# Optimization experiments

Measured on AMD Instinct MI355X. Metric: run time of the kernel, lower is better.

The kernel has to match this reference:

```python
import jax, jax.numpy as jnp
import numpy as np

D_MODEL = 2048
N_HEADS = 16
D_HEAD = D_MODEL // N_HEADS
B, S = 4, 2048


def setup_inputs() -> dict:
    key = jax.random.key(0)
    ks = jax.random.split(key, 5)
    scale = 1.0 / np.sqrt(D_MODEL)
    return {
        "x": jax.random.normal(ks[0], (B, S, D_MODEL), dtype=jnp.float32),
        "w_qkv": jax.random.normal(ks[1], (D_MODEL, 3 * D_MODEL), dtype=jnp.float32) * scale,
        "b_qkv": jax.random.normal(ks[2], (3 * D_MODEL,), dtype=jnp.float32) * 0.01,
        "w_out": jax.random.normal(ks[3], (D_MODEL, D_MODEL), dtype=jnp.float32) * scale,
        "b_out": jax.random.normal(ks[4], (D_MODEL,), dtype=jnp.float32) * 0.01,
    }


def reference(x, w_qkv, b_qkv, w_out, b_out):
    b, s, d = x.shape
    qkv = x @ w_qkv + b_qkv                      # [b, s, 3d]
    q, k, v = jnp.split(qkv, 3, axis=-1)
    # [b, h, s, dh]
    q = q.reshape(b, s, N_HEADS, D_HEAD).transpose(0, 2, 1, 3)
    k = k.reshape(b, s, N_HEADS, D_HEAD).transpose(0, 2, 1, 3)
    v = v.reshape(b, s, N_HEADS, D_HEAD).transpose(0, 2, 1, 3)
    # past_kv is None -> s_past == s
    scale = 1.0 / np.sqrt(D_HEAD).astype(np.float32)
    scores = jnp.einsum("bhqd,bhkd->bhqk", q, k) * scale  # [b, h, s, s]
    # causal mask: disallow j > i (diagonal = 1 + s_past - s = 1)
    causal = jnp.tril(jnp.ones((s, s), dtype=bool))
    scores = jnp.where(causal, scores, jnp.float32(-jnp.inf))
    attn = jax.nn.softmax(scores, axis=-1)
    out = jnp.einsum("bhqk,bhkd->bhqd", attn, v)          # [b, h, s, dh]
    out = out.transpose(0, 2, 1, 3).reshape(b, s, d)
    out = out @ w_out + b_out
    return out, k, v
```

## Files before the change

kernel.cpp:

```cpp
#include <hip/hip_runtime.h>
#include <hip/hip_bf16.h>
#include <cstdint>

typedef unsigned short u16;
typedef unsigned int u32;
typedef __attribute__((ext_vector_type(4))) float f32x4;
typedef __attribute__((ext_vector_type(8))) __bf16 bf16x8;

#define DEVFN static __device__ __forceinline__

constexpr int Bb = 4, S = 2048, Dm = 2048, H = 16, DH = 128;
constexpr int M  = Bb * S;
constexpr int N3 = 3 * Dm;
constexpr int KK = 2048;
constexpr float ATTN_SCALE = 0.088388347648318447f;
constexpr float LOG2E = 1.4426950408889634f;

DEVFN u16 f2bf(float f) {
  union { float f; u32 u; } v; v.f = f;
  u32 u = v.u;
  return (u16)((u + 0x7fffu + ((u >> 16) & 1u)) >> 16);
}

DEVFN void async16(const void* g, void* l) {
  __builtin_amdgcn_global_load_lds(
      (__attribute__((address_space(1))) unsigned int*)(g),
      (__attribute__((address_space(3))) unsigned int*)(l), 16, 0, 0);
}


__global__ __launch_bounds__(256) void k_cvt_bf16(const float* __restrict__ in,
                                                  u16* __restrict__ out, int n) {
  int i = (blockIdx.x * 256 + threadIdx.x) * 4;
  if (i < n) {
    float4 f = *(const float4*)(in + i);
    ushort4 o;
    o.x = f2bf(f.x); o.y = f2bf(f.y); o.z = f2bf(f.z); o.w = f2bf(f.w);
    *(ushort4*)(out + i) = o;
  }
}

__global__ __launch_bounds__(256) void k_transpose_bf16(const float* __restrict__ in,
                                                        u16* __restrict__ out,
                                                        int R, int C) {
  __shared__ float tile[32][33];
  int c0 = blockIdx.x * 32, r0 = blockIdx.y * 32;
  int tx = threadIdx.x & 31, ty = threadIdx.x >> 5;
#pragma unroll
  for (int i = 0; i < 4; i++)
    tile[ty + 8 * i][tx] = in[(size_t)(r0 + ty + 8 * i) * C + c0 + tx];
  __syncthreads();
#pragma unroll
  for (int i = 0; i < 4; i++)
    out[(size_t)(c0 + ty + 8 * i) * R + r0 + tx] = f2bf(tile[tx][ty + 8 * i]);
}


#define RA(buf, half) ((buf) * 65536 + (half) * 16384)
#define RB(buf, half) ((buf) * 65536 + 32768 + (half) * 16384)

#define BARRIER() __builtin_amdgcn_s_barrier()
#define LGKM12() { asm volatile("s_waitcnt lgkmcnt(12)" ::: "memory"); __builtin_amdgcn_sched_barrier(0); }
#define LGKM0()  { asm volatile("s_waitcnt lgkmcnt(0)" ::: "memory"); __builtin_amdgcn_sched_barrier(0); }
#define VMC4()   { asm volatile("s_waitcnt vmcnt(4)" ::: "memory"); __builtin_amdgcn_sched_barrier(0); }
#define VMC8()   { asm volatile("s_waitcnt vmcnt(8)" ::: "memory"); __builtin_amdgcn_sched_barrier(0); }
#define VMC0()   { asm volatile("s_waitcnt vmcnt(0)" ::: "memory"); __builtin_amdgcn_sched_barrier(0); }

template <int BUF, int QUAD>
DEVFN void ldAq(const char* lds, int wm, int lrow, int lkg, bf16x8 af[4][2]) {
  const char* base = lds + RA(BUF, 0) + wm * 16384;
  const int sw = (lrow & 7) << 4;
#pragma unroll
  for (int mi = 0; mi < 4; mi++) {
    int row = QUAD * 64 + mi * 16 + lrow;
#pragma unroll
    for (int kk = 0; kk < 2; kk++)
      af[mi][kk] = *(const bf16x8*)(base + row * 128 + ((kk * 64 + lkg * 16) ^ sw));
  }
}

template <int BUF, int NS>
DEVFN void ldB(const char* lds, int wn, int lrow, int lkg, bf16x8 b[2][2]) {
  const char* base = lds + RB(BUF, 0) + (wn >> 1) * 16384;
  const int sw = (lrow & 7) << 4;
#pragma unroll
  for (int ni = 0; ni < 2; ni++) {
    int row = (wn & 1) * 64 + NS * 32 + ni * 16 + lrow;
#pragma unroll
    for (int kk = 0; kk < 2; kk++)
      b[ni][kk] = *(const bf16x8*)(base + row * 128 + ((kk * 64 + lkg * 16) ^ sw));
  }
}

template <int MS, int NS>
DEVFN void mmq(f32x4 acc[8][4], bf16x8 af[4][2], bf16x8 b[2][2]) {
  __builtin_amdgcn_s_setprio(1);
#pragma unroll
  for (int kk = 0; kk < 2; kk++)
#pragma unroll
    for (int mi = 0; mi < 4; mi++)
#pragma unroll
      for (int ni = 0; ni < 2; ni++)
        acc[MS * 4 + mi][NS * 2 + ni] = __builtin_amdgcn_mfma_f32_16x16x32_bf16(
            af[mi][kk], b[ni][kk], acc[MS * 4 + mi][NS * 2 + ni], 0, 0, 0);
  __builtin_amdgcn_s_setprio(0);
}

DEVFN void stage2(const u16* src, char* ldsc, int region, int dstoff) {
  async16(src, ldsc + region + dstoff);
  async16(src + (size_t)64 * KK, ldsc + region + 8192 + dstoff);
}

template <int MODE>
__global__ __launch_bounds__(512, 2) void k_gemm(
    const u16* __restrict__ A, const u16* __restrict__ BT,
    const float* __restrict__ bias, float* __restrict__ Cf,
    u16* __restrict__ q_bf, u16* __restrict__ k_bf, u16* __restrict__ v_bfT,
    int N) {
  __shared__ __align__(16) char lds[131072];
  char* ldsc = lds;
  const int tid = threadIdx.x;
  const int wid = tid >> 6, lane = tid & 63;
  const int wm = wid >> 2, wn = wid & 3;
  const int lrow = lane & 15, lkg = lane >> 4;

  const int bid = blockIdx.x;
  const int xcd = bid & 7;
  const int i = bid >> 3;
  const int r = i & 15;
  const int j = i >> 4;
  const int tm0 = (xcd * 4 + (r >> 2)) << 8;
  const int tn0 = (j * 4 + (r & 3)) << 8;

  const int NT = KK >> 6;

  const int srow = tid >> 3;
  const int scol = (((tid & 7) * 16) ^ ((srow & 7) << 4)) >> 1;
  const int dstoff = (tid & ~63) * 16;
  const u16* bA0 = A + (size_t)(tm0 + srow) * KK + scol;
  const u16* bA1 = A + (size_t)(tm0 + 128 + srow) * KK + scol;
  const u16* bB0 = BT + (size_t)(tn0 + srow) * KK + scol;
  const u16* bB1 = BT + (size_t)(tn0 + 128 + srow) * KK + scol;

  f32x4 acc[8][4] = {};
  bf16x8 afX[4][2], afY[4][2], bX[2][2], bY[2][2];

  stage2(bA0, ldsc, RA(0, 0), dstoff);
  stage2(bA1, ldsc, RA(0, 1), dstoff);
  stage2(bB0, ldsc, RB(0, 0), dstoff);
  stage2(bB1, ldsc, RB(0, 1), dstoff);
  stage2(bA0 + 64, ldsc, RA(1, 0), dstoff);
  stage2(bA1 + 64, ldsc, RA(1, 1), dstoff);
  stage2(bB0 + 64, ldsc, RB(1, 0), dstoff);
  stage2(bB1 + 64, ldsc, RB(1, 1), dstoff);
  VMC8();
  BARRIER();
  ldAq<0, 0>(ldsc, wm, lrow, lkg, afX);
  ldB<0, 0>(ldsc, wn, lrow, lkg, bX);

  for (int it = 0; it < NT / 2; it++) {
    const int u = it * 2;
    const int t2 = (u + 2 < NT) ? u + 2 : NT - 2;
    const int t3 = (u + 3 < NT) ? u + 3 : NT - 1;

    ldAq<0, 1>(ldsc, wm, lrow, lkg, afY);
    ldB<0, 1>(ldsc, wn, lrow, lkg, bY);
    LGKM12();
    mmq<0, 0>(acc, afX, bX);
    LGKM0();
    BARRIER();

    stage2(bA0 + t2 * 64, ldsc, RA(0, 0), dstoff);
    stage2(bA1 + t2 * 64, ldsc, RA(0, 1), dstoff);
    mmq<0, 1>(acc, afX, bY);
    VMC4();
    BARRIER();

    ldAq<1, 0>(ldsc, wm, lrow, lkg, afX);
    stage2(bB0 + t2 * 64, ldsc, RB(0, 0), dstoff);
    mmq<1, 1>(acc, afY, bY);
    BARRIER();

    ldB<1, 0>(ldsc, wn, lrow, lkg, bY);
    stage2(bB1 + t2 * 64, ldsc, RB(0, 1), dstoff);
    mmq<1, 0>(acc, afY, bX);
    BARRIER();

    ldAq<1, 1>(ldsc, wm, lrow, lkg, afY);
    ldB<1, 1>(ldsc, wn, lrow, lkg, bX);
    LGKM12();
    mmq<0, 0>(acc, afX, bY);
    LGKM0();
    BARRIER();

    stage2(bA0 + t3 * 64, ldsc, RA(1, 0), dstoff);
    stage2(bA1 + t3 * 64, ldsc, RA(1, 1), dstoff);
    mmq<0, 1>(acc, afX, bX);
    VMC4();
    BARRIER();

    ldAq<0, 0>(ldsc, wm, lrow, lkg, afX);
    stage2(bB0 + t3 * 64, ldsc, RB(1, 0), dstoff);
    mmq<1, 1>(acc, afY, bX);
    BARRIER();

    ldB<0, 0>(ldsc, wn, lrow, lkg, bX);
    stage2(bB1 + t3 * 64, ldsc, RB(1, 1), dstoff);
    mmq<1, 0>(acc, afY, bY);
    BARRIER();
  }
  VMC0();
  LGKM0();

  if (MODE == 0) {
#pragma unroll
    for (int mig = 0; mig < 8; mig++) {
      int row = tm0 + wm * 128 + (mig >> 2) * 64 + (mig & 3) * 16 + lkg * 4;
#pragma unroll
      for (int nig = 0; nig < 4; nig++) {
        int col = tn0 + wn * 64 + (nig >> 1) * 32 + (nig & 1) * 16 + lrow;
        float bv = bias[col];
#pragma unroll
        for (int r2 = 0; r2 < 4; r2++)
          Cf[(size_t)(row + r2) * N + col] = acc[mig][nig][r2] + bv;
      }
    }
  } else {
#pragma unroll
    for (int mig = 0; mig < 8; mig++) {
      int row = tm0 + wm * 128 + (mig >> 2) * 64 + (mig & 3) * 16 + lkg * 4;
#pragma unroll
      for (int nig = 0; nig < 4; nig++) {
        int n = tn0 + wn * 64 + (nig >> 1) * 32 + (nig & 1) * 16 + lrow;
        float bv = bias[n];
        int type = n >> 11;
        int d = n & 2047;
        int h = d >> 7, dh = d & 127;
#pragma unroll
        for (int r2 = 0; r2 < 4; r2++) {
          int rr = row + r2;
          int b = rr >> 11, s = rr & 2047;
          float val = acc[mig][nig][r2] + bv;
          size_t idx = ((size_t)(b * H + h) * S + s) * DH + dh;
          if (type == 0) {
            q_bf[idx] = f2bf(val * ATTN_SCALE);
          } else if (type == 1) {
            Cf[(size_t)M * Dm + idx] = val;
            k_bf[idx] = f2bf(val);
          } else {
            Cf[(size_t)2 * M * Dm + idx] = val;
            v_bfT[((size_t)(b * H + h) * DH + dh) * S + s] = f2bf(val);
          }
        }
      }
    }
  }
}

__global__ __launch_bounds__(256, 2) void k_attn(const u16* __restrict__ q_bf,
                                                 const u16* __restrict__ k_bf,
                                                 const u16* __restrict__ v_bfT,
                                                 u16* __restrict__ attn_bf) {
  __shared__ u16 ldsK[2][64 * 128];
  __shared__ u16 ldsV[2][128 * 64];
  __shared__ u16 ldsP[4][32 * 64];

  const int tid = threadIdx.x;
  const int wid = tid >> 6, lane = tid & 63;
  const int lrow = lane & 15, lkg = lane >> 4;

  const int bid = blockIdx.x;
  const int xcd = bid & 7;
  const int ii = bid >> 3;
  const int bh = xcd * 8 + (ii >> 4);
  const int qi = 15 - (ii & 15);
  const int b = bh >> 4, h = bh & 15;
  const int wq0 = qi * 128 + wid * 32;
  const int swz = (lrow & 7) << 4;

  const u16* qp = q_bf + (size_t)bh * S * DH;
  const u16* kp = k_bf + (size_t)bh * S * DH;
  const u16* vp = v_bfT + (size_t)bh * DH * S;

  bf16x8 qf[2][4];
#pragma unroll
  for (int qt = 0; qt < 2; qt++)
#pragma unroll
    for (int kk = 0; kk < 4; kk++)
      qf[qt][kk] = *(const bf16x8*)(qp + (size_t)(wq0 + qt * 16 + lrow) * DH +
                                    kk * 32 + lkg * 8);

  float mr[2][4], lr[2][4];
#pragma unroll
  for (int qt = 0; qt < 2; qt++)
#pragma unroll
    for (int r = 0; r < 4; r++) { mr[qt][r] = -1e30f; lr[qt][r] = 0.f; }
  f32x4 oacc[2][8] = {};

  const int nkb = qi * 2 + 2;

  auto stage = [&](int kb, int buf) {
#pragma unroll
    for (int i = 0; i < 4; i++) {
      int L = i * 4096 + wid * 1024 + lane * 16;
      int krow = L >> 8, kch = (L >> 4) & 15;
      async16(kp + (size_t)(kb * 64 + krow) * DH + ((kch ^ (krow & 7)) * 8),
              (char*)ldsK[buf] + L);
      int vd = L >> 7, vch = (L >> 4) & 7;
      async16(vp + (size_t)vd * S + kb * 64 + ((vch ^ (vd & 7)) * 8),
              (char*)ldsV[buf] + L);
    }
  };

  stage(0, 0);
  asm volatile("s_waitcnt vmcnt(0)" ::: "memory");
  __builtin_amdgcn_s_barrier();

  int cur = 0;
  for (int kb = 0; kb < nkb; kb++) {
    if (kb + 1 < nkb) stage(kb + 1, cur ^ 1);

    if (kb * 64 <= wq0 + 31) {
      const u16* Kc = ldsK[cur];
      const u16* Vc = ldsV[cur];
      f32x4 sacc[2][4] = {};
      __builtin_amdgcn_s_setprio(1);
#pragma unroll
      for (int kt = 0; kt < 4; kt++)
#pragma unroll
        for (int kk = 0; kk < 4; kk++) {
          bf16x8 kf = *(const bf16x8*)((const char*)Kc +
                        (kt * 16 + lrow) * 256 + ((kk * 64 + lkg * 16) ^ swz));
          sacc[0][kt] = __builtin_amdgcn_mfma_f32_16x16x32_bf16(qf[0][kk], kf,
                                                                sacc[0][kt], 0, 0, 0);
          sacc[1][kt] = __builtin_amdgcn_mfma_f32_16x16x32_bf16(qf[1][kk], kf,
                                                                sacc[1][kt], 0, 0, 0);
        }
      __builtin_amdgcn_s_setprio(0);

      if (kb * 64 + 63 > wq0) {
#pragma unroll
        for (int qt = 0; qt < 2; qt++)
#pragma unroll
          for (int kt = 0; kt < 4; kt++) {
            int k = kb * 64 + kt * 16 + lrow;
#pragma unroll
            for (int r = 0; r < 4; r++)
              if (k > wq0 + qt * 16 + lkg * 4 + r) sacc[qt][kt][r] = -1e30f;
          }
      }

      float pm[2][4];
#pragma unroll
      for (int qt = 0; qt < 2; qt++)
#pragma unroll
        for (int r = 0; r < 4; r++)
          pm[qt][r] = fmaxf(fmaxf(sacc[qt][0][r], sacc[qt][1][r]),
                            fmaxf(sacc[qt][2][r], sacc[qt][3][r]));
#pragma unroll
      for (int off = 1; off < 16; off <<= 1)
#pragma unroll
        for (int qt = 0; qt < 2; qt++)
#pragma unroll
          for (int r = 0; r < 4; r++)
            pm[qt][r] = fmaxf(pm[qt][r], __shfl_xor(pm[qt][r], off, 64));

      float dmax = pm[0][0] - mr[0][0];
#pragma unroll
      for (int qt = 0; qt < 2; qt++)
#pragma unroll
        for (int r = 0; r < 4; r++)
          dmax = fmaxf(dmax, pm[qt][r] - mr[qt][r]);
      if (!__all(dmax <= 8.0f)) {
        float sc[2][4];
#pragma unroll
        for (int qt = 0; qt < 2; qt++)
#pragma unroll
          for (int r = 0; r < 4; r++) {
            float mn = fmaxf(mr[qt][r], pm[qt][r]);
            sc[qt][r] = exp2f((mr[qt][r] - mn) * LOG2E);
            mr[qt][r] = mn;
            lr[qt][r] *= sc[qt][r];
          }
#pragma unroll
        for (int qt = 0; qt < 2; qt++)
#pragma unroll
          for (int nd = 0; nd < 8; nd++)
#pragma unroll
            for (int r = 0; r < 4; r++) oacc[qt][nd][r] *= sc[qt][r];
      }

      float rs[2][4] = {};
#pragma unroll
      for (int qt = 0; qt < 2; qt++)
#pragma unroll
        for (int kt = 0; kt < 4; kt++)
#pragma unroll
          for (int r = 0; r < 4; r++) {
            float p = exp2f((sacc[qt][kt][r] - mr[qt][r]) * LOG2E);
            rs[qt][r] += p;
            int prow = qt * 16 + lkg * 4 + r;
            *(u16*)((char*)ldsP[wid] + prow * 128 +
                    (((kt * 16 + lrow) * 2) ^ ((prow & 7) << 4))) = f2bf(p);
          }
#pragma unroll
      for (int off = 1; off < 16; off <<= 1)
#pragma unroll
        for (int qt = 0; qt < 2; qt++)
#pragma unroll
          for (int r = 0; r < 4; r++)
            rs[qt][r] += __shfl_xor(rs[qt][r], off, 64);
#pragma unroll
      for (int qt = 0; qt < 2; qt++)
#pragma unroll
        for (int r = 0; r < 4; r++)
          lr[qt][r] += rs[qt][r];

      asm volatile("s_waitcnt lgkmcnt(0)" ::: "memory");
      bf16x8 pf[2][2];
#pragma unroll
      for (int qt = 0; qt < 2; qt++)
#pragma unroll
        for (int kk = 0; kk < 2; kk++)
          pf[qt][kk] = *(const bf16x8*)((const char*)ldsP[wid] +
                         (qt * 16 + lrow) * 128 + ((kk * 64 + lkg * 16) ^ swz));
      __builtin_amdgcn_s_setprio(1);
#pragma unroll
      for (int nd = 0; nd < 8; nd++) {
        bf16x8 vf0 = *(const bf16x8*)((const char*)Vc +
                       (nd * 16 + lrow) * 128 + ((lkg * 16) ^ swz));
        bf16x8 vf1 = *(const bf16x8*)((const char*)Vc +
                       (nd * 16 + lrow) * 128 + ((64 + lkg * 16) ^ swz));
#pragma unroll
        for (int qt = 0; qt < 2; qt++) {
          oacc[qt][nd] = __builtin_amdgcn_mfma_f32_16x16x32_bf16(pf[qt][0], vf0,
                                                                 oacc[qt][nd], 0, 0, 0);
          oacc[qt][nd] = __builtin_amdgcn_mfma_f32_16x16x32_bf16(pf[qt][1], vf1,
                                                                 oacc[qt][nd], 0, 0, 0);
        }
      }
      __builtin_amdgcn_s_setprio(0);
    }

    asm volatile("s_waitcnt vmcnt(0)" ::: "memory");
    __builtin_amdgcn_s_barrier();
    cur ^= 1;
  }

#pragma unroll
  for (int qt = 0; qt < 2; qt++) {
    float inv[4];
#pragma unroll
    for (int r = 0; r < 4; r++) inv[r] = 1.0f / lr[qt][r];
#pragma unroll
    for (int nd = 0; nd < 8; nd++)
#pragma unroll
      for (int r = 0; r < 4; r++) {
        int q = wq0 + qt * 16 + lkg * 4 + r;
        size_t idx = ((size_t)(b * S + q) * H + h) * DH + nd * 16 + lrow;
        attn_bf[idx] = f2bf(oacc[qt][nd][r] * inv[r]);
      }
  }
}


extern "C" void kernel_launch(void* const* d_in, const int* in_sizes, int n_in,
                              void* d_out, int out_size, void* d_ws, size_t ws_size,
                              hipStream_t stream) {
  const float* x     = (const float*)d_in[0];
  const float* w_qkv = (const float*)d_in[1];
  const float* b_qkv = (const float*)d_in[2];
  const float* w_out = (const float*)d_in[3];
  const float* b_out = (const float*)d_in[4];
  float* out = (float*)d_out;

  char* ws = (char*)d_ws;
  u16* x_bf    = (u16*)ws; ws += (size_t)M * Dm * 2;
  u16* wqkvT   = (u16*)ws; ws += (size_t)N3 * Dm * 2;
  u16* woutT   = (u16*)ws; ws += (size_t)Dm * Dm * 2;
  u16* q_bf    = (u16*)ws; ws += (size_t)M * Dm * 2;
  u16* k_bf    = (u16*)ws; ws += (size_t)M * Dm * 2;
  u16* v_bfT   = (u16*)ws; ws += (size_t)M * Dm * 2;
  u16* attn_bf = (u16*)ws; ws += (size_t)M * Dm * 2;

  k_cvt_bf16<<<(M * Dm) / 1024, 256, 0, stream>>>(x, x_bf, M * Dm);
  k_transpose_bf16<<<dim3(N3 / 32, Dm / 32), 256, 0, stream>>>(w_qkv, wqkvT, Dm, N3);
  k_transpose_bf16<<<dim3(Dm / 32, Dm / 32), 256, 0, stream>>>(w_out, woutT, Dm, Dm);

  k_gemm<1><<<(N3 / 256) * (M / 256), 512, 0, stream>>>(
      x_bf, wqkvT, b_qkv, out, q_bf, k_bf, v_bfT, N3);

  k_attn<<<S / 128 * Bb * H, 256, 0, stream>>>(q_bf, k_bf, v_bfT, attn_bf);

  k_gemm<0><<<(Dm / 256) * (M / 256), 512, 0, stream>>>(
      attn_bf, woutT, b_out, out, nullptr, nullptr, nullptr, Dm);
}
```

Baseline: 565.7 us.

## Restructure GEMM main loop into finer-grained quarter-tile staged pipeline

Rewrites the GEMM K-loop schedule so each global-to-LDS async load is issued one quarter-tile at a time, interleaved with eight MFMA phases per double iteration. It uses tighter vmcnt(2) waits and full lgkmcnt(0) waits between barrier pairs, instead of the previous lgkmcnt(12)/vmcnt(4) scheme with register prefetch across phases. The goal is smoother overlap of global loads with compute. The trade-off is many more barriers per iteration and less LDS-read to MFMA overlap, which could stall the waves.

```diff
diff --git a/kernel.cpp b/kernel.cpp
--- a/kernel.cpp
+++ b/kernel.cpp
@@ -60,11 +60,9 @@
 #define RB(buf, half) ((buf) * 65536 + 32768 + (half) * 16384)
 
 #define BARRIER() __builtin_amdgcn_s_barrier()
-#define LGKM12() { asm volatile("s_waitcnt lgkmcnt(12)" ::: "memory"); __builtin_amdgcn_sched_barrier(0); }
-#define LGKM0()  { asm volatile("s_waitcnt lgkmcnt(0)" ::: "memory"); __builtin_amdgcn_sched_barrier(0); }
-#define VMC4()   { asm volatile("s_waitcnt vmcnt(4)" ::: "memory"); __builtin_amdgcn_sched_barrier(0); }
-#define VMC8()   { asm volatile("s_waitcnt vmcnt(8)" ::: "memory"); __builtin_amdgcn_sched_barrier(0); }
-#define VMC0()   { asm volatile("s_waitcnt vmcnt(0)" ::: "memory"); __builtin_amdgcn_sched_barrier(0); }
+#define LGK0() { asm volatile("s_waitcnt lgkmcnt(0)" ::: "memory"); __builtin_amdgcn_sched_barrier(0); }
+#define VMC2() { asm volatile("s_waitcnt vmcnt(2)" ::: "memory"); __builtin_amdgcn_sched_barrier(0); }
+#define VMC0() { asm volatile("s_waitcnt vmcnt(0)" ::: "memory"); __builtin_amdgcn_sched_barrier(0); }
 
 template <int BUF, int QUAD>
 DEVFN void ldAq(const char* lds, int wm, int lrow, int lkg, bf16x8 af[4][2]) {
@@ -104,11 +102,6 @@
         acc[MS * 4 + mi][NS * 2 + ni] = __builtin_amdgcn_mfma_f32_16x16x32_bf16(
             af[mi][kk], b[ni][kk], acc[MS * 4 + mi][NS * 2 + ni], 0, 0, 0);
   __builtin_amdgcn_s_setprio(0);
-}
-
-DEVFN void stage2(const u16* src, char* ldsc, int region, int dstoff) {
-  async16(src, ldsc + region + dstoff);
-  async16(src + (size_t)64 * KK, ldsc + region + 8192 + dstoff);
 }
 
 template <int MODE>
@@ -142,75 +135,79 @@
   const u16* bB0 = BT + (size_t)(tn0 + srow) * KK + scol;
   const u16* bB1 = BT + (size_t)(tn0 + 128 + srow) * KK + scol;
 
+  auto stage2 = [&](const u16* src, int region) {
+    async16(src, ldsc + region + dstoff);
+    async16(src + (size_t)64 * KK, ldsc + region + 8192 + dstoff);
+  };
+
   f32x4 acc[8][4] = {};
-  bf16x8 afX[4][2], afY[4][2], bX[2][2], bY[2][2];
-
-  stage2(bA0, ldsc, RA(0, 0), dstoff);
-  stage2(bA1, ldsc, RA(0, 1), dstoff);
-  stage2(bB0, ldsc, RB(0, 0), dstoff);
-  stage2(bB1, ldsc, RB(0, 1), dstoff);
-  stage2(bA0 + 64, ldsc, RA(1, 0), dstoff);
-  stage2(bA1 + 64, ldsc, RA(1, 1), dstoff);
-  stage2(bB0 + 64, ldsc, RB(1, 0), dstoff);
-  stage2(bB1 + 64, ldsc, RB(1, 1), dstoff);
-  VMC8();
+  bf16x8 afA[4][2], afB[4][2], b0[2][2], b1[2][2];
+
+  stage2(bA0, RA(0, 0));
+  stage2(bA1, RA(0, 1));
+  stage2(bB0, RB(0, 0));
+  stage2(bB1, RB(0, 1));
+  stage2(bA0 + 64, RA(1, 0));
+  VMC2();
   BARRIER();
-  ldAq<0, 0>(ldsc, wm, lrow, lkg, afX);
-  ldB<0, 0>(ldsc, wn, lrow, lkg, bX);
 
   for (int it = 0; it < NT / 2; it++) {
-    const int u = it * 2;
-    const int t2 = (u + 2 < NT) ? u + 2 : NT - 2;
-    const int t3 = (u + 3 < NT) ? u + 3 : NT - 1;
-
-    ldAq<0, 1>(ldsc, wm, lrow, lkg, afY);
-    ldB<0, 1>(ldsc, wn, lrow, lkg, bY);
-    LGKM12();
-    mmq<0, 0>(acc, afX, bX);
-    LGKM0();
-    BARRIER();
-
-    stage2(bA0 + t2 * 64, ldsc, RA(0, 0), dstoff);
-    stage2(bA1 + t2 * 64, ldsc, RA(0, 1), dstoff);
-    mmq<0, 1>(acc, afX, bY);
-    VMC4();
-    BARRIER();
-
-    ldAq<1, 0>(ldsc, wm, lrow, lkg, afX);
-    stage2(bB0 + t2 * 64, ldsc, RB(0, 0), dstoff);
-    mmq<1, 1>(acc, afY, bY);
-    BARRIER();
-
-    ldB<1, 0>(ldsc, wn, lrow, lkg, bY);
-    stage2(bB1 + t2 * 64, ldsc, RB(0, 1), dstoff);
-    mmq<1, 0>(acc, afY, bX);
-    BARRIER();
-
-    ldAq<1, 1>(ldsc, wm, lrow, lkg, afY);
-    ldB<1, 1>(ldsc, wn, lrow, lkg, bX);
-    LGKM12();
-    mmq<0, 0>(acc, afX, bY);
-    LGKM0();
-    BARRIER();
-
-    stage2(bA0 + t3 * 64, ldsc, RA(1, 0), dstoff);
-    stage2(bA1 + t3 * 64, ldsc, RA(1, 1), dstoff);
-    mmq<0, 1>(acc, afX, bX);
-    VMC4();
-    BARRIER();
-
-    ldAq<0, 0>(ldsc, wm, lrow, lkg, afX);
-    stage2(bB0 + t3 * 64, ldsc, RB(1, 0), dstoff);
-    mmq<1, 1>(acc, afY, bX);
-    BARRIER();
-
-    ldB<0, 0>(ldsc, wn, lrow, lkg, bX);
-    stage2(bB1 + t3 * 64, ldsc, RB(1, 1), dstoff);
-    mmq<1, 0>(acc, afY, bY);
+    const int t = 2 * it;
+    const int t1 = (t + 1) * 64;
+    const int t2 = (t + 2 < NT) ? (t + 2) * 64 : 0;
+    const int t3 = (t + 3 < NT) ? (t + 3) * 64 : 0;
+
+    ldAq<0, 0>(ldsc, wm, lrow, lkg, afA);
+    ldB<0, 0>(ldsc, wn, lrow, lkg, b0);
+    stage2(bA1 + t1, RA(1, 1));
+    BARRIER(); LGK0();
+    mmq<0, 0>(acc, afA, b0);
+    BARRIER();
+
+    ldB<0, 1>(ldsc, wn, lrow, lkg, b1);
+    stage2(bB0 + t1, RB(1, 0));
+    BARRIER(); LGK0();
+    mmq<0, 1>(acc, afA, b1);
+    BARRIER();
+
+    ldAq<0, 1>(ldsc, wm, lrow, lkg, afB);
+    stage2(bB1 + t1, RB(1, 1));
+    BARRIER(); LGK0();
+    mmq<1, 1>(acc, afB, b1);
+    BARRIER();
+
+    stage2(bA0 + t2, RA(0, 0));
+    VMC2();
+    BARRIER();
+    mmq<1, 0>(acc, afB, b0);
+    BARRIER();
+
+    ldAq<1, 0>(ldsc, wm, lrow, lkg, afA);
+    ldB<1, 0>(ldsc, wn, lrow, lkg, b0);
+    stage2(bA1 + t2, RA(0, 1));
+    BARRIER(); LGK0();
+    mmq<0, 0>(acc, afA, b0);
+    BARRIER();
+
+    ldB<1, 1>(ldsc, wn, lrow, lkg, b1);
+    stage2(bB0 + t2, RB(0, 0));
+    BARRIER(); LGK0();
+    mmq<0, 1>(acc, afA, b1);
+    BARRIER();
+
+    ldAq<1, 1>(ldsc, wm, lrow, lkg, afB);
+    stage2(bB1 + t2, RB(0, 1));
+    BARRIER(); LGK0();
+    mmq<1, 1>(acc, afB, b1);
+    BARRIER();
+
+    stage2(bA0 + t3, RA(1, 0));
+    VMC2();
+    BARRIER();
+    mmq<1, 0>(acc, afB, b0);
     BARRIER();
   }
   VMC0();
-  LGKM0();
 
   if (MODE == 0) {
 #pragma unroll
```

New measurement: 552.0 us. 1.02x faster.
